# Kernel tuning notes

Measured on AMD Instinct MI355X. Metric: run time of the kernel, lower is better.

The kernel has to match this reference:

```python
import jax, jax.numpy as jnp
import numpy as np
import math

B, N = 512, 32
OBS, NA = 128, 16
OA = OBS + NA  # 144
DK = 64


def setup_inputs() -> dict:
    key = jax.random.key(0)
    ks = jax.random.split(key, 12)
    return {
        "states": jax.random.normal(ks[0], (B, N, OBS), jnp.float32),
        "policies": jax.random.uniform(ks[1], (B, N, NA), jnp.float32),
        "actions": jax.random.uniform(ks[2], (B, N, NA), jnp.float32),
        "W_obs": jax.random.normal(ks[3], (64, OBS), jnp.float32) * 0.05,
        "b_obs": jax.random.normal(ks[4], (64,), jnp.float32) * 0.05,
        "W_oa": jax.random.normal(ks[5], (64, OA), jnp.float32) * 0.05,
        "b_oa": jax.random.normal(ks[6], (64,), jnp.float32) * 0.05,
        "W_key": jax.random.normal(ks[7], (DK, 64), jnp.float32) * 0.05,
        "W_query": jax.random.normal(ks[8], (DK, 64), jnp.float32) * 0.05,
        "W_attn_val": jax.random.normal(ks[9], (64, 64), jnp.float32) * 0.05,
        "W_f1": jax.random.normal(ks[10], (64, 64), jnp.float32) * 0.05,
        "W_f2": jax.random.normal(ks[11], (16, 64), jnp.float32) * 0.05,
    }


def reference(states, policies, actions, W_obs, b_obs, W_oa, b_oa,
              W_key, W_query, W_attn_val, W_f1, W_f2):
    num_agents = states.shape[1]
    d_k = W_attn_val.shape[0]  # d_k_obs == obs_act_output_dim

    obs_actions = jnp.concatenate([states, actions], axis=-1)   # [B,N,OA]
    obs_policy = jnp.concatenate([states, policies], axis=-1)   # [B,N,OA]

    states_embed = jax.nn.relu(states @ W_obs.T + b_obs)        # [B,N,64]
    key_obs = states_embed @ W_key.T                            # [B,N,DK]
    query_obs = states_embed @ W_query.T                        # [B,N,DK]

    # score after transpose(1,2): score[b,j,i] = q_i . k_j ; softmax over i
    score = jnp.einsum('bid,bjd->bji', query_obs, key_obs)
    weight = jax.nn.softmax(score / math.sqrt(d_k), axis=-1)    # [B,N,N]

    # mixed input: for row j, entry i uses policy if i==j else action
    eye = jnp.eye(num_agents, dtype=states.dtype)[None, :, :, None]  # [1,N,N,1]
    oap = eye * obs_policy[:, None, :, :] + (1.0 - eye) * obs_actions[:, None, :, :]  # [B,N,N,OA]

    emb = jax.nn.relu(oap @ W_oa.T + b_oa)                      # [B,N,N,64]
    attn_vals = jnp.tanh(emb @ W_attn_val.T)                    # [B,N,N,64]

    node_features = jnp.mean(attn_vals * weight[..., None], axis=2)  # [B,N,64]

    value = jax.nn.leaky_relu(node_features @ W_f1.T)           # slope 0.01, matches torch default
    value = value @ W_f2.T                                      # [B,N,16]
    return value, weight
```

## Files before the change

kernel.cpp:

```cpp
#include <hip/hip_runtime.h>

typedef _Float16 f16;
typedef _Float16 f16x8 __attribute__((ext_vector_type(8)));
typedef float f32x4 __attribute__((ext_vector_type(4)));

#define MFMA16(a, b, c) __builtin_amdgcn_mfma_f32_16x16x32_f16((a), (b), (c), 0, 0, 0)

#define WS_OBS 0
#define WS_OA  16384
#define WS_K   36864
#define WS_Q   45056
#define WS_AV  53248
#define WS_F1  61440
#define WS_F2  69632
#define WS_TOT 71680

#define XS_HI  0
#define XS_LO  4352
#define E_HI   8704
#define E_LO   11008
#define EA_HI  13312
#define EA_LO  15616
#define EP_HI  17920
#define EP_LO  20224
#define KB_HI  22528
#define KB_LO  24832
#define QB_HI  27136
#define QB_LO  29440
#define AAT_HI 31744
#define AAT_LO 34304
#define WM_HI  36864
#define WM_LO  38144
#define WDIAG  39424
#define SMTOT  39488

__device__ __forceinline__ void split1(float v, ushort& h, ushort& lo) {
    f16 hf = (f16)v;
    float r = v - (float)hf;
    f16 lf = (f16)r;
    union { f16 f; ushort u; } a, b;
    a.f = hf; b.f = lf;
    h = a.u; lo = b.u;
}
__device__ __forceinline__ void split4(f32x4 v, ushort4& h, ushort4& l) {
    split1(v[0], h.x, l.x);
    split1(v[1], h.y, l.y);
    split1(v[2], h.z, l.z);
    split1(v[3], h.w, l.w);
}
__device__ __forceinline__ void mk8(float4 a, float4 b, f16x8& hi, f16x8& lo) {
    float v[8] = {a.x, a.y, a.z, a.w, b.x, b.y, b.z, b.w};
    #pragma unroll
    for (int j = 0; j < 8; ++j) {
        f16 h = (f16)v[j];
        hi[j] = h;
        lo[j] = (f16)(v[j] - (float)h);
    }
}
__device__ __forceinline__ f16x8 ldf(const ushort* sm, int off) {
    return *(const f16x8*)(sm + off);
}
__device__ __forceinline__ f16x8 ldw(const f16* wsf, int base, int psz, int nch,
                                     int p, int nt, int c, int l) {
    return *(const f16x8*)(wsf + base + p * psz + (((nt * nch + c) << 6) + l) * 8);
}
__device__ __forceinline__ float fast_tanh(float x) {
    float xc = fminf(fmaxf(x, -9.0f), 9.0f);
    float e = __expf(2.0f * xc);
    return (e - 1.0f) * __builtin_amdgcn_rcpf(e + 1.0f);
}

__global__ void prep_frags(const float* __restrict__ Wobs, const float* __restrict__ Woa,
                           const float* __restrict__ Wk,   const float* __restrict__ Wq,
                           const float* __restrict__ Wav,  const float* __restrict__ Wf1,
                           const float* __restrict__ Wf2,  f16* __restrict__ wsf) {
    int tid = blockIdx.x * 256 + threadIdx.x;
    if (tid >= 8960) return;
    int p = tid >= 4480 ? 1 : 0;
    int g = tid - p * 4480;
    const float* W; int base, psz, nch, Kreal, g0;
    if (g < 1024)      { W = Wobs; base = WS_OBS; psz = 8192;  nch = 4; Kreal = 128; g0 = g; }
    else if (g < 2304) { W = Woa;  base = WS_OA;  psz = 10240; nch = 5; Kreal = 144; g0 = g - 1024; }
    else if (g < 2816) { W = Wk;   base = WS_K;   psz = 4096;  nch = 2; Kreal = 64;  g0 = g - 2304; }
    else if (g < 3328) { W = Wq;   base = WS_Q;   psz = 4096;  nch = 2; Kreal = 64;  g0 = g - 2816; }
    else if (g < 3840) { W = Wav;  base = WS_AV;  psz = 4096;  nch = 2; Kreal = 64;  g0 = g - 3328; }
    else if (g < 4352) { W = Wf1;  base = WS_F1;  psz = 4096;  nch = 2; Kreal = 64;  g0 = g - 3840; }
    else               { W = Wf2;  base = WS_F2;  psz = 1024;  nch = 2; Kreal = 64;  g0 = g - 4352; }
    int l = g0 & 63, fc = g0 >> 6;
    int c = fc % nch, nt = fc / nch;
    int o = nt * 16 + (l & 15);
    int k0 = c * 32 + (l >> 4) * 8;
    f16 out[8];
    #pragma unroll
    for (int j = 0; j < 8; ++j) {
        int k = k0 + j;
        float v = (k < Kreal) ? W[o * Kreal + k] : 0.0f;
        f16 h = (f16)v;
        out[j] = p ? (f16)(v - (float)h) : h;
    }
    *(f16x8*)(wsf + base + p * psz + g0 * 8) = *(f16x8*)out;
}

__global__ void __launch_bounds__(256, 2)
critic_mfma(const float* __restrict__ states, const float* __restrict__ policies,
            const float* __restrict__ actions, const float* __restrict__ b_obs,
            const float* __restrict__ b_oa, const f16* __restrict__ wsf,
            float* __restrict__ out_value,
            float* __restrict__ out_weight)
{
    __shared__ ushort sm[SMTOT];
    const int b = blockIdx.x;
    const int t = threadIdx.x;
    const int wv = t >> 6, l = t & 63;
    const int lr = l & 15;
    const int lg = l >> 4;
    const int ft = wv;
    const int f0 = ft * 16 + lg * 4;

    float4 sv[4];
    {
        const float4* src = (const float4*)(states + (size_t)b * 4096);
        #pragma unroll
        for (int r4 = 0; r4 < 4; ++r4) sv[r4] = src[t + r4 * 256];
    }

    f16x8 wObsH[4], wObsL[4], wOaH[4], wOaL[4];
    #pragma unroll
    for (int c = 0; c < 4; ++c) {
        wObsH[c] = ldw(wsf, WS_OBS, 8192, 4, 0, ft, c, l);
        wObsL[c] = ldw(wsf, WS_OBS, 8192, 4, 1, ft, c, l);
        wOaH[c]  = ldw(wsf, WS_OA, 10240, 5, 0, ft, c, l);
        wOaL[c]  = ldw(wsf, WS_OA, 10240, 5, 1, ft, c, l);
    }
    f16x8 wTailH = ldw(wsf, WS_OA, 10240, 5, 0, ft, 4, l);
    f16x8 wTailL = ldw(wsf, WS_OA, 10240, 5, 1, ft, 4, l);

    f16x8 actH[2], actL[2], polH[2], polL[2];
    #pragma unroll
    for (int at = 0; at < 2; ++at) {
        float4 a0v = make_float4(0.f, 0.f, 0.f, 0.f), a1v = a0v, p0v = a0v, p1v = a0v;
        if (lg < 2) {
            size_t base = (size_t)b * 512 + (at * 16 + lr) * 16 + lg * 8;
            a0v = *(const float4*)(actions + base);
            a1v = *(const float4*)(actions + base + 4);
            p0v = *(const float4*)(policies + base);
            p1v = *(const float4*)(policies + base + 4);
        }
        mk8(a0v, a1v, actH[at], actL[at]);
        mk8(p0v, p1v, polH[at], polL[at]);
    }

    #pragma unroll
    for (int r4 = 0; r4 < 4; ++r4) {
        int e4 = t + r4 * 256, row = e4 >> 5, k0 = (e4 & 31) * 4;
        ushort4 h, lo;
        split1(sv[r4].x, h.x, lo.x);
        split1(sv[r4].y, h.y, lo.y);
        split1(sv[r4].z, h.z, lo.z);
        split1(sv[r4].w, h.w, lo.w);
        *(ushort4*)(sm + XS_HI + row * 136 + k0) = h;
        *(ushort4*)(sm + XS_LO + row * 136 + k0) = lo;
    }
    __syncthreads();

    const f32x4 Z = {0.f, 0.f, 0.f, 0.f};

    f32x4 accE[2] = {Z, Z}, accP[2] = {Z, Z};
    #pragma unroll
    for (int c = 0; c < 4; ++c) {
        #pragma unroll
        for (int at = 0; at < 2; ++at) {
            int ao = (at * 16 + lr) * 136 + c * 32 + lg * 8;
            f16x8 xh = ldf(sm, XS_HI + ao), xl = ldf(sm, XS_LO + ao);
            accE[at] = MFMA16(wObsH[c], xh, accE[at]);
            accE[at] = MFMA16(wObsH[c], xl, accE[at]);
            accE[at] = MFMA16(wObsL[c], xh, accE[at]);
            accP[at] = MFMA16(wOaH[c], xh, accP[at]);
            accP[at] = MFMA16(wOaH[c], xl, accP[at]);
            accP[at] = MFMA16(wOaL[c], xh, accP[at]);
        }
    }
    f32x4 accEA[2], accEP[2];
    #pragma unroll
    for (int at = 0; at < 2; ++at) {
        accEA[at] = accP[at]; accEP[at] = accP[at];
        accEA[at] = MFMA16(wTailH, actH[at], accEA[at]);
        accEA[at] = MFMA16(wTailH, actL[at], accEA[at]);
        accEA[at] = MFMA16(wTailL, actH[at], accEA[at]);
        accEP[at] = MFMA16(wTailH, polH[at], accEP[at]);
        accEP[at] = MFMA16(wTailH, polL[at], accEP[at]);
        accEP[at] = MFMA16(wTailL, polH[at], accEP[at]);
    }

    f16x8 wKH[2], wKL[2], wQH[2], wQL[2], wVH[2], wVL[2];
    #pragma unroll
    for (int c = 0; c < 2; ++c) {
        wKH[c] = ldw(wsf, WS_K, 4096, 2, 0, ft, c, l);
        wKL[c] = ldw(wsf, WS_K, 4096, 2, 1, ft, c, l);
        wQH[c] = ldw(wsf, WS_Q, 4096, 2, 0, ft, c, l);
        wQL[c] = ldw(wsf, WS_Q, 4096, 2, 1, ft, c, l);
        wVH[c] = ldw(wsf, WS_AV, 4096, 2, 0, ft, c, l);
        wVL[c] = ldw(wsf, WS_AV, 4096, 2, 1, ft, c, l);
    }

    {
        float4 bo = *(const float4*)&b_obs[f0];
        float4 ba = *(const float4*)&b_oa[f0];
        #pragma unroll
        for (int at = 0; at < 2; ++at) {
            int agent = at * 16 + lr;
            f32x4 e, ea, ep;
            e[0] = fmaxf(accE[at][0] + bo.x, 0.f);  e[1] = fmaxf(accE[at][1] + bo.y, 0.f);
            e[2] = fmaxf(accE[at][2] + bo.z, 0.f);  e[3] = fmaxf(accE[at][3] + bo.w, 0.f);
            ea[0] = fmaxf(accEA[at][0] + ba.x, 0.f); ea[1] = fmaxf(accEA[at][1] + ba.y, 0.f);
            ea[2] = fmaxf(accEA[at][2] + ba.z, 0.f); ea[3] = fmaxf(accEA[at][3] + ba.w, 0.f);
            ep[0] = fmaxf(accEP[at][0] + ba.x, 0.f); ep[1] = fmaxf(accEP[at][1] + ba.y, 0.f);
            ep[2] = fmaxf(accEP[at][2] + ba.z, 0.f); ep[3] = fmaxf(accEP[at][3] + ba.w, 0.f);
            ushort4 h, lo;
            split4(e, h, lo);
            *(ushort4*)(sm + E_HI + agent * 72 + f0) = h;
            *(ushort4*)(sm + E_LO + agent * 72 + f0) = lo;
            split4(ea, h, lo);
            *(ushort4*)(sm + EA_HI + agent * 72 + f0) = h;
            *(ushort4*)(sm + EA_LO + agent * 72 + f0) = lo;
            split4(ep, h, lo);
            *(ushort4*)(sm + EP_HI + agent * 72 + f0) = h;
            *(ushort4*)(sm + EP_LO + agent * 72 + f0) = lo;
        }
    }
    __syncthreads();

    f32x4 dDiff[2];
    {
        f32x4 aK[2] = {Z, Z}, aQ[2] = {Z, Z}, aA[2] = {Z, Z}, aP[2] = {Z, Z};
        #pragma unroll
        for (int c = 0; c < 2; ++c) {
            #pragma unroll
            for (int at = 0; at < 2; ++at) {
                int ao = (at * 16 + lr) * 72 + c * 32 + lg * 8;
                f16x8 eh = ldf(sm, E_HI + ao),  el = ldf(sm, E_LO + ao);
                f16x8 xh = ldf(sm, EA_HI + ao), xl = ldf(sm, EA_LO + ao);
                f16x8 yh = ldf(sm, EP_HI + ao), yl = ldf(sm, EP_LO + ao);
                aK[at] = MFMA16(wKH[c], eh, aK[at]);
                aK[at] = MFMA16(wKH[c], el, aK[at]);
                aK[at] = MFMA16(wKL[c], eh, aK[at]);
                aQ[at] = MFMA16(wQH[c], eh, aQ[at]);
                aQ[at] = MFMA16(wQH[c], el, aQ[at]);
                aQ[at] = MFMA16(wQL[c], eh, aQ[at]);
                aA[at] = MFMA16(wVH[c], xh, aA[at]);
                aA[at] = MFMA16(wVH[c], xl, aA[at]);
                aA[at] = MFMA16(wVL[c], xh, aA[at]);
                aP[at] = MFMA16(wVH[c], yh, aP[at]);
                aP[at] = MFMA16(wVH[c], yl, aP[at]);
                aP[at] = MFMA16(wVL[c], yh, aP[at]);
            }
        }
        #pragma unroll
        for (int at = 0; at < 2; ++at) {
            int agent = at * 16 + lr;
            ushort4 h, lo;
            split4(aK[at], h, lo);
            *(ushort4*)(sm + KB_HI + agent * 72 + f0) = h;
            *(ushort4*)(sm + KB_LO + agent * 72 + f0) = lo;
            split4(aQ[at], h, lo);
            *(ushort4*)(sm + QB_HI + agent * 72 + f0) = h;
            *(ushort4*)(sm + QB_LO + agent * 72 + f0) = lo;
            f32x4 ta, tp;
            #pragma unroll
            for (int r = 0; r < 4; ++r) {
                ta[r] = fast_tanh(aA[at][r]);
                tp[r] = fast_tanh(aP[at][r]);
            }
            dDiff[at] = tp - ta;
            #pragma unroll
            for (int r = 0; r < 4; ++r) {
                ushort hh, ll;
                split1(ta[r], hh, ll);
                sm[AAT_HI + (f0 + r) * 40 + agent] = hh;
                sm[AAT_LO + (f0 + r) * 40 + agent] = ll;
            }
        }
    }

    f16x8 wF1H[2], wF1L[2], wF2H[2], wF2L[2];
    #pragma unroll
    for (int c = 0; c < 2; ++c) {
        wF1H[c] = ldw(wsf, WS_F1, 4096, 2, 0, ft, c, l);
        wF1L[c] = ldw(wsf, WS_F1, 4096, 2, 1, ft, c, l);
    }
    if (wv < 2) {
        #pragma unroll
        for (int c = 0; c < 2; ++c) {
            wF2H[c] = ldw(wsf, WS_F2, 1024, 2, 0, 0, c, l);
            wF2L[c] = ldw(wsf, WS_F2, 1024, 2, 1, 0, c, l);
        }
    }
    __syncthreads();

    if (wv < 2) {
        int jt = wv;
        f16x8 kh[2], kl[2];
        #pragma unroll
        for (int c = 0; c < 2; ++c) {
            int ko = (jt * 16 + lr) * 72 + c * 32 + lg * 8;
            kh[c] = ldf(sm, KB_HI + ko);
            kl[c] = ldf(sm, KB_LO + ko);
        }
        f32x4 s[2] = {Z, Z};
        #pragma unroll
        for (int c = 0; c < 2; ++c) {
            #pragma unroll
            for (int it = 0; it < 2; ++it) {
                int qo = (it * 16 + lr) * 72 + c * 32 + lg * 8;
                f16x8 qh = ldf(sm, QB_HI + qo), ql = ldf(sm, QB_LO + qo);
                s[it] = MFMA16(kh[c], qh, s[it]);
                s[it] = MFMA16(kh[c], ql, s[it]);
                s[it] = MFMA16(kl[c], qh, s[it]);
            }
        }
        float* wdiag = (float*)(sm + WDIAG);
        #pragma unroll
        for (int r = 0; r < 4; ++r) {
            int j = jt * 16 + lg * 4 + r;
            float v0 = s[0][r] * 0.125f, v1 = s[1][r] * 0.125f;
            float m = fmaxf(v0, v1);
            #pragma unroll
            for (int off = 1; off < 16; off <<= 1)
                m = fmaxf(m, __shfl_xor(m, off, 16));
            float e0 = __expf(v0 - m), e1 = __expf(v1 - m);
            float su = e0 + e1;
            #pragma unroll
            for (int off = 1; off < 16; off <<= 1)
                su += __shfl_xor(su, off, 16);
            float inv = 1.0f / su;
            e0 *= inv; e1 *= inv;
            out_weight[(size_t)b * 1024 + j * 32 + lr] = e0;
            out_weight[(size_t)b * 1024 + j * 32 + 16 + lr] = e1;
            ushort hh, ll;
            split1(e0, hh, ll);
            sm[WM_HI + j * 40 + lr] = hh;
            sm[WM_LO + j * 40 + lr] = ll;
            split1(e1, hh, ll);
            sm[WM_HI + j * 40 + 16 + lr] = hh;
            sm[WM_LO + j * 40 + 16 + lr] = ll;
            if (lr == lg * 4 + r) wdiag[j] = jt ? e1 : e0;
        }
    }
    __syncthreads();

    {
        int fo = (ft * 16 + lr) * 40 + lg * 8;
        f16x8 ah = ldf(sm, AAT_HI + fo);
        f16x8 al = ldf(sm, AAT_LO + fo);
        const float* wdiag = (const float*)(sm + WDIAG);
        #pragma unroll
        for (int jt = 0; jt < 2; ++jt) {
            int j = jt * 16 + lr;
            f16x8 wh = ldf(sm, WM_HI + j * 40 + lg * 8);
            f16x8 wl = ldf(sm, WM_LO + j * 40 + lg * 8);
            f32x4 acc = Z;
            acc = MFMA16(ah, wh, acc);
            acc = MFMA16(ah, wl, acc);
            acc = MFMA16(al, wh, acc);
            float wd = wdiag[j];
            f32x4 nf;
            #pragma unroll
            for (int r = 0; r < 4; ++r)
                nf[r] = (acc[r] + wd * dDiff[jt][r]) * 0.03125f;
            ushort4 h, lo;
            split4(nf, h, lo);
            *(ushort4*)(sm + E_HI + j * 72 + f0) = h;
            *(ushort4*)(sm + E_LO + j * 72 + f0) = lo;
        }
    }
    __syncthreads();

    {
        f32x4 hA[2] = {Z, Z};
        #pragma unroll
        for (int c = 0; c < 2; ++c) {
            #pragma unroll
            for (int jt = 0; jt < 2; ++jt) {
                int bo2 = (jt * 16 + lr) * 72 + c * 32 + lg * 8;
                f16x8 nh_ = ldf(sm, E_HI + bo2), nl_ = ldf(sm, E_LO + bo2);
                hA[jt] = MFMA16(wF1H[c], nh_, hA[jt]);
                hA[jt] = MFMA16(wF1H[c], nl_, hA[jt]);
                hA[jt] = MFMA16(wF1L[c], nh_, hA[jt]);
            }
        }
        #pragma unroll
        for (int jt = 0; jt < 2; ++jt) {
            int j = jt * 16 + lr;
            f32x4 hv;
            #pragma unroll
            for (int r = 0; r < 4; ++r)
                hv[r] = fmaxf(hA[jt][r], 0.01f * hA[jt][r]);
            ushort4 h, lo;
            split4(hv, h, lo);
            *(ushort4*)(sm + EA_HI + j * 72 + f0) = h;
            *(ushort4*)(sm + EA_LO + j * 72 + f0) = lo;
        }
    }
    __syncthreads();

    if (wv < 2) {
        int jt = wv;
        f32x4 acc = Z;
        #pragma unroll
        for (int c = 0; c < 2; ++c) {
            int ho = (jt * 16 + lr) * 72 + c * 32 + lg * 8;
            f16x8 hh = ldf(sm, EA_HI + ho), hl = ldf(sm, EA_LO + ho);
            acc = MFMA16(wF2H[c], hh, acc);
            acc = MFMA16(wF2H[c], hl, acc);
            acc = MFMA16(wF2L[c], hh, acc);
        }
        int j = jt * 16 + lr;
        *(float4*)&out_value[(size_t)b * 512 + j * 16 + lg * 4] =
            make_float4(acc[0], acc[1], acc[2], acc[3]);
    }
}

extern "C" void kernel_launch(void* const* d_in, const int* in_sizes, int n_in,
                              void* d_out, int out_size, void* d_ws, size_t ws_size,
                              hipStream_t stream) {
    const float* states   = (const float*)d_in[0];
    const float* policies = (const float*)d_in[1];
    const float* actions  = (const float*)d_in[2];
    const float* W_obs    = (const float*)d_in[3];
    const float* b_obs    = (const float*)d_in[4];
    const float* W_oa     = (const float*)d_in[5];
    const float* b_oa     = (const float*)d_in[6];
    const float* W_key    = (const float*)d_in[7];
    const float* W_query  = (const float*)d_in[8];
    const float* W_av     = (const float*)d_in[9];
    const float* W_f1     = (const float*)d_in[10];
    const float* W_f2     = (const float*)d_in[11];

    f16* wsf = (f16*)d_ws;
    float* out_value  = (float*)d_out;
    float* out_weight = (float*)d_out + 512 * 32 * 16;

    prep_frags<<<35, 256, 0, stream>>>(W_obs, W_oa, W_key, W_query, W_av, W_f1, W_f2, wsf);
    critic_mfma<<<512, 256, 0, stream>>>(states, policies, actions,
                                         b_obs, b_oa, wsf, out_value, out_weight);
}
```

Before: 20.57 us.

## Pack two batch elements per 512-thread block with overlapped LDS arenas

Each block now processes two batch elements, one per 256-thread half, with 256 blocks of 512 threads instead of 512 blocks of 256. The shared-memory layout is reorganised so later buffers (K/Q/AAT etc.) alias the input staging area, shrinking each half's arena. The first projection's MFMA chains are split into two independent accumulators per output to shorten dependency chains. Risks: launch_bounds(512,2) tightens register limits and may cause spills, and block-wide barriers now couple two independent batch items.

```diff
diff --git a/kernel.cpp b/kernel.cpp
--- a/kernel.cpp
+++ b/kernel.cpp
@@ -17,22 +17,23 @@
 
 #define XS_HI  0
 #define XS_LO  4352
-#define E_HI   8704
-#define E_LO   11008
-#define EA_HI  13312
-#define EA_LO  15616
-#define EP_HI  17920
-#define EP_LO  20224
-#define KB_HI  22528
-#define KB_LO  24832
-#define QB_HI  27136
-#define QB_LO  29440
-#define AAT_HI 31744
-#define AAT_LO 34304
-#define WM_HI  36864
-#define WM_LO  38144
-#define WDIAG  39424
-#define SMTOT  39488
+#define KB_HI  0
+#define KB_LO  2304
+#define QB_HI  4608
+#define QB_LO  6912
+#define AAT_HI 9216
+#define AAT_LO 11776
+#define E_HI   14336
+#define E_LO   16640
+#define EA_HI  18944
+#define EA_LO  21248
+#define EP_HI  23552
+#define EP_LO  25856
+#define WM_HI  28160
+#define WM_LO  29440
+#define WDIAG  30720
+#define ARENA  30784
+#define SMTOT  (2 * ARENA)
 
 __device__ __forceinline__ void split1(float v, ushort& h, ushort& lo) {
     f16 hf = (f16)v;
@@ -101,27 +102,30 @@
     *(f16x8*)(wsf + base + p * psz + g0 * 8) = *(f16x8*)out;
 }
 
-__global__ void __launch_bounds__(256, 2)
+__global__ void __launch_bounds__(512, 2)
 critic_mfma(const float* __restrict__ states, const float* __restrict__ policies,
             const float* __restrict__ actions, const float* __restrict__ b_obs,
             const float* __restrict__ b_oa, const f16* __restrict__ wsf,
             float* __restrict__ out_value,
             float* __restrict__ out_weight)
 {
-    __shared__ ushort sm[SMTOT];
-    const int b = blockIdx.x;
+    __shared__ ushort smraw[SMTOT];
     const int t = threadIdx.x;
     const int wv = t >> 6, l = t & 63;
+    const int bt = t >> 8;
+    const int tb = t & 255;
+    const int ft = wv & 3;
     const int lr = l & 15;
     const int lg = l >> 4;
-    const int ft = wv;
     const int f0 = ft * 16 + lg * 4;
+    const int b = blockIdx.x * 2 + bt;
+    ushort* sm = smraw + bt * ARENA;
 
     float4 sv[4];
     {
         const float4* src = (const float4*)(states + (size_t)b * 4096);
         #pragma unroll
-        for (int r4 = 0; r4 < 4; ++r4) sv[r4] = src[t + r4 * 256];
+        for (int r4 = 0; r4 < 4; ++r4) sv[r4] = src[tb + r4 * 256];
     }
 
     f16x8 wObsH[4], wObsL[4], wOaH[4], wOaL[4];
@@ -152,7 +156,7 @@
 
     #pragma unroll
     for (int r4 = 0; r4 < 4; ++r4) {
-        int e4 = t + r4 * 256, row = e4 >> 5, k0 = (e4 & 31) * 4;
+        int e4 = tb + r4 * 256, row = e4 >> 5, k0 = (e4 & 31) * 4;
         ushort4 h, lo;
         split1(sv[r4].x, h.x, lo.x);
         split1(sv[r4].y, h.y, lo.y);
@@ -165,25 +169,37 @@
 
     const f32x4 Z = {0.f, 0.f, 0.f, 0.f};
 
-    f32x4 accE[2] = {Z, Z}, accP[2] = {Z, Z};
+    f32x4 accEa[2] = {Z, Z}, accEb[2] = {Z, Z}, accPa[2] = {Z, Z}, accPb[2] = {Z, Z};
     #pragma unroll
     for (int c = 0; c < 4; ++c) {
         #pragma unroll
         for (int at = 0; at < 2; ++at) {
             int ao = (at * 16 + lr) * 136 + c * 32 + lg * 8;
             f16x8 xh = ldf(sm, XS_HI + ao), xl = ldf(sm, XS_LO + ao);
-            accE[at] = MFMA16(wObsH[c], xh, accE[at]);
-            accE[at] = MFMA16(wObsH[c], xl, accE[at]);
-            accE[at] = MFMA16(wObsL[c], xh, accE[at]);
-            accP[at] = MFMA16(wOaH[c], xh, accP[at]);
-            accP[at] = MFMA16(wOaH[c], xl, accP[at]);
-            accP[at] = MFMA16(wOaL[c], xh, accP[at]);
-        }
-    }
-    f32x4 accEA[2], accEP[2];
+            if ((c & 1) == 0) {
+                accEa[at] = MFMA16(wObsH[c], xh, accEa[at]);
+                accEa[at] = MFMA16(wObsH[c], xl, accEa[at]);
+                accEa[at] = MFMA16(wObsL[c], xh, accEa[at]);
+                accPa[at] = MFMA16(wOaH[c], xh, accPa[at]);
+                accPa[at] = MFMA16(wOaH[c], xl, accPa[at]);
+                accPa[at] = MFMA16(wOaL[c], xh, accPa[at]);
+            } else {
+                accEb[at] = MFMA16(wObsH[c], xh, accEb[at]);
+                accEb[at] = MFMA16(wObsH[c], xl, accEb[at]);
+                accEb[at] = MFMA16(wObsL[c], xh, accEb[at]);
+                accPb[at] = MFMA16(wOaH[c], xh, accPb[at]);
+                accPb[at] = MFMA16(wOaH[c], xl, accPb[at]);
+                accPb[at] = MFMA16(wOaL[c], xh, accPb[at]);
+            }
+        }
+    }
+    f32x4 accE[2], accEA[2], accEP[2];
     #pragma unroll
     for (int at = 0; at < 2; ++at) {
-        accEA[at] = accP[at]; accEP[at] = accP[at];
+        accE[at] = accEa[at] + accEb[at];
+        f32x4 base = accPa[at] + accPb[at];
+        accEA[at] = base;
+        accEP[at] = base;
         accEA[at] = MFMA16(wTailH, actH[at], accEA[at]);
         accEA[at] = MFMA16(wTailH, actL[at], accEA[at]);
         accEA[at] = MFMA16(wTailL, actH[at], accEA[at]);
@@ -288,7 +304,7 @@
         wF1H[c] = ldw(wsf, WS_F1, 4096, 2, 0, ft, c, l);
         wF1L[c] = ldw(wsf, WS_F1, 4096, 2, 1, ft, c, l);
     }
-    if (wv < 2) {
+    if (ft < 2) {
         #pragma unroll
         for (int c = 0; c < 2; ++c) {
             wF2H[c] = ldw(wsf, WS_F2, 1024, 2, 0, 0, c, l);
@@ -297,8 +313,8 @@
     }
     __syncthreads();
 
-    if (wv < 2) {
-        int jt = wv;
+    if (ft < 2) {
+        int jt = ft;
         f16x8 kh[2], kl[2];
         #pragma unroll
         for (int c = 0; c < 2; ++c) {
@@ -403,8 +419,8 @@
     }
     __syncthreads();
 
-    if (wv < 2) {
-        int jt = wv;
+    if (ft < 2) {
+        int jt = ft;
         f32x4 acc = Z;
         #pragma unroll
         for (int c = 0; c < 2; ++c) {
@@ -441,6 +457,6 @@
     float* out_weight = (float*)d_out + 512 * 32 * 16;
 
     prep_frags<<<35, 256, 0, stream>>>(W_obs, W_oa, W_key, W_query, W_av, W_f1, W_f2, wsf);
-    critic_mfma<<<512, 256, 0, stream>>>(states, policies, actions,
+    critic_mfma<<<256, 512, 0, stream>>>(states, policies, actions,
                                          b_obs, b_oa, wsf, out_value, out_weight);
 }
```

Result: slower. 21.09 us (+2.5%).

## Merge weight prep into a single-wave-per-batch critic kernel

Applied to the files above, without the earlier changes.

Removes the separate prep_frags launch and instead loads fp32 weights directly in the main kernel, splitting them into hi/lo fp16 fragments on the fly. Each batch element is now handled by one 64-thread wave that loops over the four feature tiles, in place of four waves. States are loaded straight into registers instead of being staged through shared memory, which shrinks LDS use. This trades a kernel launch and several barriers for more serial work per wave, repeated weight conversion in every block, and lower parallelism per block.

```diff
diff --git a/kernel.cpp b/kernel.cpp
--- a/kernel.cpp
+++ b/kernel.cpp
@@ -6,33 +6,22 @@
 
 #define MFMA16(a, b, c) __builtin_amdgcn_mfma_f32_16x16x32_f16((a), (b), (c), 0, 0, 0)
 
-#define WS_OBS 0
-#define WS_OA  16384
-#define WS_K   36864
-#define WS_Q   45056
-#define WS_AV  53248
-#define WS_F1  61440
-#define WS_F2  69632
-#define WS_TOT 71680
-
-#define XS_HI  0
-#define XS_LO  4352
-#define E_HI   8704
-#define E_LO   11008
-#define EA_HI  13312
-#define EA_LO  15616
-#define EP_HI  17920
-#define EP_LO  20224
-#define KB_HI  22528
-#define KB_LO  24832
-#define QB_HI  27136
-#define QB_LO  29440
-#define AAT_HI 31744
-#define AAT_LO 34304
-#define WM_HI  36864
-#define WM_LO  38144
-#define WDIAG  39424
-#define SMTOT  39488
+#define E_HI   0
+#define E_LO   2304
+#define EA_HI  4608
+#define EA_LO  6912
+#define EP_HI  9216
+#define EP_LO  11520
+#define KB_HI  13824
+#define KB_LO  16128
+#define QB_HI  18432
+#define QB_LO  20736
+#define AAT_HI 23040
+#define AAT_LO 25600
+#define WM_HI  28160
+#define WM_LO  29440
+#define WDIAG  30720
+#define SMTOT  30784
 
 __device__ __forceinline__ void split1(float v, ushort& h, ushort& lo) {
     f16 hf = (f16)v;
@@ -57,12 +46,13 @@
         lo[j] = (f16)(v[j] - (float)h);
     }
 }
+__device__ __forceinline__ void ldraw(const float* p, f16x8& h, f16x8& l) {
+    float4 a = *(const float4*)p;
+    float4 b = *(const float4*)(p + 4);
+    mk8(a, b, h, l);
+}
 __device__ __forceinline__ f16x8 ldf(const ushort* sm, int off) {
     return *(const f16x8*)(sm + off);
-}
-__device__ __forceinline__ f16x8 ldw(const f16* wsf, int base, int psz, int nch,
-                                     int p, int nt, int c, int l) {
-    return *(const f16x8*)(wsf + base + p * psz + (((nt * nch + c) << 6) + l) * 8);
 }
 __device__ __forceinline__ float fast_tanh(float x) {
     float xc = fminf(fmaxf(x, -9.0f), 9.0f);
@@ -70,70 +60,31 @@
     return (e - 1.0f) * __builtin_amdgcn_rcpf(e + 1.0f);
 }
 
-__global__ void prep_frags(const float* __restrict__ Wobs, const float* __restrict__ Woa,
-                           const float* __restrict__ Wk,   const float* __restrict__ Wq,
-                           const float* __restrict__ Wav,  const float* __restrict__ Wf1,
-                           const float* __restrict__ Wf2,  f16* __restrict__ wsf) {
-    int tid = blockIdx.x * 256 + threadIdx.x;
-    if (tid >= 8960) return;
-    int p = tid >= 4480 ? 1 : 0;
-    int g = tid - p * 4480;
-    const float* W; int base, psz, nch, Kreal, g0;
-    if (g < 1024)      { W = Wobs; base = WS_OBS; psz = 8192;  nch = 4; Kreal = 128; g0 = g; }
-    else if (g < 2304) { W = Woa;  base = WS_OA;  psz = 10240; nch = 5; Kreal = 144; g0 = g - 1024; }
-    else if (g < 2816) { W = Wk;   base = WS_K;   psz = 4096;  nch = 2; Kreal = 64;  g0 = g - 2304; }
-    else if (g < 3328) { W = Wq;   base = WS_Q;   psz = 4096;  nch = 2; Kreal = 64;  g0 = g - 2816; }
-    else if (g < 3840) { W = Wav;  base = WS_AV;  psz = 4096;  nch = 2; Kreal = 64;  g0 = g - 3328; }
-    else if (g < 4352) { W = Wf1;  base = WS_F1;  psz = 4096;  nch = 2; Kreal = 64;  g0 = g - 3840; }
-    else               { W = Wf2;  base = WS_F2;  psz = 1024;  nch = 2; Kreal = 64;  g0 = g - 4352; }
-    int l = g0 & 63, fc = g0 >> 6;
-    int c = fc % nch, nt = fc / nch;
-    int o = nt * 16 + (l & 15);
-    int k0 = c * 32 + (l >> 4) * 8;
-    f16 out[8];
-    #pragma unroll
-    for (int j = 0; j < 8; ++j) {
-        int k = k0 + j;
-        float v = (k < Kreal) ? W[o * Kreal + k] : 0.0f;
-        f16 h = (f16)v;
-        out[j] = p ? (f16)(v - (float)h) : h;
-    }
-    *(f16x8*)(wsf + base + p * psz + g0 * 8) = *(f16x8*)out;
-}
-
-__global__ void __launch_bounds__(256, 2)
-critic_mfma(const float* __restrict__ states, const float* __restrict__ policies,
-            const float* __restrict__ actions, const float* __restrict__ b_obs,
-            const float* __restrict__ b_oa, const f16* __restrict__ wsf,
-            float* __restrict__ out_value,
-            float* __restrict__ out_weight)
+__global__ void __launch_bounds__(64, 1)
+critic_one(const float* __restrict__ states, const float* __restrict__ policies,
+           const float* __restrict__ actions, const float* __restrict__ b_obs,
+           const float* __restrict__ b_oa,
+           const float* __restrict__ W_obs, const float* __restrict__ W_oa,
+           const float* __restrict__ W_key, const float* __restrict__ W_query,
+           const float* __restrict__ W_av,  const float* __restrict__ W_f1,
+           const float* __restrict__ W_f2,
+           float* __restrict__ out_value,
+           float* __restrict__ out_weight)
 {
     __shared__ ushort sm[SMTOT];
     const int b = blockIdx.x;
-    const int t = threadIdx.x;
-    const int wv = t >> 6, l = t & 63;
+    const int l = threadIdx.x;
     const int lr = l & 15;
     const int lg = l >> 4;
-    const int ft = wv;
-    const int f0 = ft * 16 + lg * 4;
-
-    float4 sv[4];
-    {
-        const float4* src = (const float4*)(states + (size_t)b * 4096);
-        #pragma unroll
-        for (int r4 = 0; r4 < 4; ++r4) sv[r4] = src[t + r4 * 256];
-    }
-
-    f16x8 wObsH[4], wObsL[4], wOaH[4], wOaL[4];
-    #pragma unroll
-    for (int c = 0; c < 4; ++c) {
-        wObsH[c] = ldw(wsf, WS_OBS, 8192, 4, 0, ft, c, l);
-        wObsL[c] = ldw(wsf, WS_OBS, 8192, 4, 1, ft, c, l);
-        wOaH[c]  = ldw(wsf, WS_OA, 10240, 5, 0, ft, c, l);
-        wOaL[c]  = ldw(wsf, WS_OA, 10240, 5, 1, ft, c, l);
-    }
-    f16x8 wTailH = ldw(wsf, WS_OA, 10240, 5, 0, ft, 4, l);
-    f16x8 wTailL = ldw(wsf, WS_OA, 10240, 5, 1, ft, 4, l);
+    const f32x4 Z = {0.f, 0.f, 0.f, 0.f};
+
+    f16x8 sxh[2][4], sxl[2][4];
+    #pragma unroll
+    for (int at = 0; at < 2; ++at)
+        #pragma unroll
+        for (int c = 0; c < 4; ++c)
+            ldraw(states + (size_t)b * 4096 + (at * 16 + lr) * 128 + c * 32 + lg * 8,
+                  sxh[at][c], sxl[at][c]);
 
     f16x8 actH[2], actL[2], polH[2], polL[2];
     #pragma unroll
@@ -151,71 +102,56 @@
     }
 
     #pragma unroll
-    for (int r4 = 0; r4 < 4; ++r4) {
-        int e4 = t + r4 * 256, row = e4 >> 5, k0 = (e4 & 31) * 4;
-        ushort4 h, lo;
-        split1(sv[r4].x, h.x, lo.x);
-        split1(sv[r4].y, h.y, lo.y);
-        split1(sv[r4].z, h.z, lo.z);
-        split1(sv[r4].w, h.w, lo.w);
-        *(ushort4*)(sm + XS_HI + row * 136 + k0) = h;
-        *(ushort4*)(sm + XS_LO + row * 136 + k0) = lo;
-    }
-    __syncthreads();
-
-    const f32x4 Z = {0.f, 0.f, 0.f, 0.f};
-
-    f32x4 accE[2] = {Z, Z}, accP[2] = {Z, Z};
-    #pragma unroll
-    for (int c = 0; c < 4; ++c) {
-        #pragma unroll
-        for (int at = 0; at < 2; ++at) {
-            int ao = (at * 16 + lr) * 136 + c * 32 + lg * 8;
-            f16x8 xh = ldf(sm, XS_HI + ao), xl = ldf(sm, XS_LO + ao);
-            accE[at] = MFMA16(wObsH[c], xh, accE[at]);
-            accE[at] = MFMA16(wObsH[c], xl, accE[at]);
-            accE[at] = MFMA16(wObsL[c], xh, accE[at]);
-            accP[at] = MFMA16(wOaH[c], xh, accP[at]);
-            accP[at] = MFMA16(wOaH[c], xl, accP[at]);
-            accP[at] = MFMA16(wOaL[c], xh, accP[at]);
-        }
-    }
-    f32x4 accEA[2], accEP[2];
-    #pragma unroll
-    for (int at = 0; at < 2; ++at) {
-        accEA[at] = accP[at]; accEP[at] = accP[at];
-        accEA[at] = MFMA16(wTailH, actH[at], accEA[at]);
-        accEA[at] = MFMA16(wTailH, actL[at], accEA[at]);
-        accEA[at] = MFMA16(wTailL, actH[at], accEA[at]);
-        accEP[at] = MFMA16(wTailH, polH[at], accEP[at]);
-        accEP[at] = MFMA16(wTailH, polL[at], accEP[at]);
-        accEP[at] = MFMA16(wTailL, polH[at], accEP[at]);
-    }
-
-    f16x8 wKH[2], wKL[2], wQH[2], wQL[2], wVH[2], wVL[2];
-    #pragma unroll
-    for (int c = 0; c < 2; ++c) {
-        wKH[c] = ldw(wsf, WS_K, 4096, 2, 0, ft, c, l);
-        wKL[c] = ldw(wsf, WS_K, 4096, 2, 1, ft, c, l);
-        wQH[c] = ldw(wsf, WS_Q, 4096, 2, 0, ft, c, l);
-        wQL[c] = ldw(wsf, WS_Q, 4096, 2, 1, ft, c, l);
-        wVH[c] = ldw(wsf, WS_AV, 4096, 2, 0, ft, c, l);
-        wVL[c] = ldw(wsf, WS_AV, 4096, 2, 1, ft, c, l);
-    }
-
-    {
+    for (int ft = 0; ft < 4; ++ft) {
+        const int row = ft * 16 + lr;
+        const int f0 = ft * 16 + lg * 4;
+        f16x8 oh[4], ol[4], ah[4], al[4];
+        #pragma unroll
+        for (int c = 0; c < 4; ++c) {
+            ldraw(W_obs + row * 128 + c * 32 + lg * 8, oh[c], ol[c]);
+            ldraw(W_oa + row * 144 + c * 32 + lg * 8, ah[c], al[c]);
+        }
+        f16x8 th, tl;
+        {
+            float4 t0 = make_float4(0.f, 0.f, 0.f, 0.f), t1 = t0;
+            if (lg < 2) {
+                t0 = *(const float4*)(W_oa + row * 144 + 128 + lg * 8);
+                t1 = *(const float4*)(W_oa + row * 144 + 132 + lg * 8);
+            }
+            mk8(t0, t1, th, tl);
+        }
+        f32x4 accE[2] = {Z, Z}, accP[2] = {Z, Z};
+        #pragma unroll
+        for (int c = 0; c < 4; ++c) {
+            #pragma unroll
+            for (int at = 0; at < 2; ++at) {
+                accE[at] = MFMA16(oh[c], sxh[at][c], accE[at]);
+                accE[at] = MFMA16(oh[c], sxl[at][c], accE[at]);
+                accE[at] = MFMA16(ol[c], sxh[at][c], accE[at]);
+                accP[at] = MFMA16(ah[c], sxh[at][c], accP[at]);
+                accP[at] = MFMA16(ah[c], sxl[at][c], accP[at]);
+                accP[at] = MFMA16(al[c], sxh[at][c], accP[at]);
+            }
+        }
         float4 bo = *(const float4*)&b_obs[f0];
         float4 ba = *(const float4*)&b_oa[f0];
         #pragma unroll
         for (int at = 0; at < 2; ++at) {
+            f32x4 accA = accP[at], accQ = accP[at];
+            accA = MFMA16(th, actH[at], accA);
+            accA = MFMA16(th, actL[at], accA);
+            accA = MFMA16(tl, actH[at], accA);
+            accQ = MFMA16(th, polH[at], accQ);
+            accQ = MFMA16(th, polL[at], accQ);
+            accQ = MFMA16(tl, polH[at], accQ);
             int agent = at * 16 + lr;
             f32x4 e, ea, ep;
             e[0] = fmaxf(accE[at][0] + bo.x, 0.f);  e[1] = fmaxf(accE[at][1] + bo.y, 0.f);
             e[2] = fmaxf(accE[at][2] + bo.z, 0.f);  e[3] = fmaxf(accE[at][3] + bo.w, 0.f);
-            ea[0] = fmaxf(accEA[at][0] + ba.x, 0.f); ea[1] = fmaxf(accEA[at][1] + ba.y, 0.f);
-            ea[2] = fmaxf(accEA[at][2] + ba.z, 0.f); ea[3] = fmaxf(accEA[at][3] + ba.w, 0.f);
-            ep[0] = fmaxf(accEP[at][0] + ba.x, 0.f); ep[1] = fmaxf(accEP[at][1] + ba.y, 0.f);
-            ep[2] = fmaxf(accEP[at][2] + ba.z, 0.f); ep[3] = fmaxf(accEP[at][3] + ba.w, 0.f);
+            ea[0] = fmaxf(accA[0] + ba.x, 0.f); ea[1] = fmaxf(accA[1] + ba.y, 0.f);
+            ea[2] = fmaxf(accA[2] + ba.z, 0.f); ea[3] = fmaxf(accA[3] + ba.w, 0.f);
+            ep[0] = fmaxf(accQ[0] + ba.x, 0.f); ep[1] = fmaxf(accQ[1] + ba.y, 0.f);
+            ep[2] = fmaxf(accQ[2] + ba.z, 0.f); ep[3] = fmaxf(accQ[3] + ba.w, 0.f);
             ushort4 h, lo;
             split4(e, h, lo);
             *(ushort4*)(sm + E_HI + agent * 72 + f0) = h;
@@ -230,29 +166,46 @@
     }
     __syncthreads();
 
-    f32x4 dDiff[2];
-    {
+    f16x8 beh[2][2], bel[2][2], bxh[2][2], bxl[2][2], byh[2][2], byl[2][2];
+    #pragma unroll
+    for (int at = 0; at < 2; ++at)
+        #pragma unroll
+        for (int c = 0; c < 2; ++c) {
+            int ao = (at * 16 + lr) * 72 + c * 32 + lg * 8;
+            beh[at][c] = ldf(sm, E_HI + ao);  bel[at][c] = ldf(sm, E_LO + ao);
+            bxh[at][c] = ldf(sm, EA_HI + ao); bxl[at][c] = ldf(sm, EA_LO + ao);
+            byh[at][c] = ldf(sm, EP_HI + ao); byl[at][c] = ldf(sm, EP_LO + ao);
+        }
+
+    f32x4 dDiff[4][2];
+    #pragma unroll
+    for (int ft = 0; ft < 4; ++ft) {
+        const int row = ft * 16 + lr;
+        const int f0 = ft * 16 + lg * 4;
+        f16x8 kh[2], kl[2], qh[2], ql[2], vh[2], vl[2];
+        #pragma unroll
+        for (int c = 0; c < 2; ++c) {
+            ldraw(W_key + row * 64 + c * 32 + lg * 8, kh[c], kl[c]);
+            ldraw(W_query + row * 64 + c * 32 + lg * 8, qh[c], ql[c]);
+            ldraw(W_av + row * 64 + c * 32 + lg * 8, vh[c], vl[c]);
+        }
         f32x4 aK[2] = {Z, Z}, aQ[2] = {Z, Z}, aA[2] = {Z, Z}, aP[2] = {Z, Z};
         #pragma unroll
         for (int c = 0; c < 2; ++c) {
             #pragma unroll
             for (int at = 0; at < 2; ++at) {
-                int ao = (at * 16 + lr) * 72 + c * 32 + lg * 8;
-                f16x8 eh = ldf(sm, E_HI + ao),  el = ldf(sm, E_LO + ao);
-                f16x8 xh = ldf(sm, EA_HI + ao), xl = ldf(sm, EA_LO + ao);
-                f16x8 yh = ldf(sm, EP_HI + ao), yl = ldf(sm, EP_LO + ao);
-                aK[at] = MFMA16(wKH[c], eh, aK[at]);
-                aK[at] = MFMA16(wKH[c], el, aK[at]);
-                aK[at] = MFMA16(wKL[c], eh, aK[at]);
-                aQ[at] = MFMA16(wQH[c], eh, aQ[at]);
-                aQ[at] = MFMA16(wQH[c], el, aQ[at]);
-                aQ[at] = MFMA16(wQL[c], eh, aQ[at]);
-                aA[at] = MFMA16(wVH[c], xh, aA[at]);
-                aA[at] = MFMA16(wVH[c], xl, aA[at]);
-                aA[at] = MFMA16(wVL[c], xh, aA[at]);
-                aP[at] = MFMA16(wVH[c], yh, aP[at]);
-                aP[at] = MFMA16(wVH[c], yl, aP[at]);
-                aP[at] = MFMA16(wVL[c], yh, aP[at]);
+                aK[at] = MFMA16(kh[c], beh[at][c], aK[at]);
+                aK[at] = MFMA16(kh[c], bel[at][c], aK[at]);
+                aK[at] = MFMA16(kl[c], beh[at][c], aK[at]);
+                aQ[at] = MFMA16(qh[c], beh[at][c], aQ[at]);
+                aQ[at] = MFMA16(qh[c], bel[at][c], aQ[at]);
+                aQ[at] = MFMA16(ql[c], beh[at][c], aQ[at]);
+                aA[at] = MFMA16(vh[c], bxh[at][c], aA[at]);
+                aA[at] = MFMA16(vh[c], bxl[at][c], aA[at]);
+                aA[at] = MFMA16(vl[c], bxh[at][c], aA[at]);
+                aP[at] = MFMA16(vh[c], byh[at][c], aP[at]);
+                aP[at] = MFMA16(vh[c], byl[at][c], aP[at]);
+                aP[at] = MFMA16(vl[c], byh[at][c], aP[at]);
             }
         }
         #pragma unroll
@@ -271,7 +224,7 @@
                 ta[r] = fast_tanh(aA[at][r]);
                 tp[r] = fast_tanh(aP[at][r]);
             }
-            dDiff[at] = tp - ta;
+            dDiff[ft][at] = tp - ta;
             #pragma unroll
             for (int r = 0; r < 4; ++r) {
                 ushort hh, ll;
@@ -281,142 +234,161 @@
             }
         }
     }
-
-    f16x8 wF1H[2], wF1L[2], wF2H[2], wF2L[2];
-    #pragma unroll
-    for (int c = 0; c < 2; ++c) {
-        wF1H[c] = ldw(wsf, WS_F1, 4096, 2, 0, ft, c, l);
-        wF1L[c] = ldw(wsf, WS_F1, 4096, 2, 1, ft, c, l);
-    }
-    if (wv < 2) {
-        #pragma unroll
-        for (int c = 0; c < 2; ++c) {
-            wF2H[c] = ldw(wsf, WS_F2, 1024, 2, 0, 0, c, l);
-            wF2L[c] = ldw(wsf, WS_F2, 1024, 2, 1, 0, c, l);
-        }
-    }
     __syncthreads();
 
-    if (wv < 2) {
-        int jt = wv;
-        f16x8 kh[2], kl[2];
-        #pragma unroll
-        for (int c = 0; c < 2; ++c) {
-            int ko = (jt * 16 + lr) * 72 + c * 32 + lg * 8;
-            kh[c] = ldf(sm, KB_HI + ko);
-            kl[c] = ldf(sm, KB_LO + ko);
-        }
-        f32x4 s[2] = {Z, Z};
-        #pragma unroll
-        for (int c = 0; c < 2; ++c) {
-            #pragma unroll
-            for (int it = 0; it < 2; ++it) {
-                int qo = (it * 16 + lr) * 72 + c * 32 + lg * 8;
-                f16x8 qh = ldf(sm, QB_HI + qo), ql = ldf(sm, QB_LO + qo);
-                s[it] = MFMA16(kh[c], qh, s[it]);
-                s[it] = MFMA16(kh[c], ql, s[it]);
-                s[it] = MFMA16(kl[c], qh, s[it]);
-            }
-        }
+    {
         float* wdiag = (float*)(sm + WDIAG);
         #pragma unroll
-        for (int r = 0; r < 4; ++r) {
-            int j = jt * 16 + lg * 4 + r;
-            float v0 = s[0][r] * 0.125f, v1 = s[1][r] * 0.125f;
-            float m = fmaxf(v0, v1);
-            #pragma unroll
-            for (int off = 1; off < 16; off <<= 1)
-                m = fmaxf(m, __shfl_xor(m, off, 16));
-            float e0 = __expf(v0 - m), e1 = __expf(v1 - m);
-            float su = e0 + e1;
-            #pragma unroll
-            for (int off = 1; off < 16; off <<= 1)
-                su += __shfl_xor(su, off, 16);
-            float inv = 1.0f / su;
-            e0 *= inv; e1 *= inv;
-            out_weight[(size_t)b * 1024 + j * 32 + lr] = e0;
-            out_weight[(size_t)b * 1024 + j * 32 + 16 + lr] = e1;
-            ushort hh, ll;
-            split1(e0, hh, ll);
-            sm[WM_HI + j * 40 + lr] = hh;
-            sm[WM_LO + j * 40 + lr] = ll;
-            split1(e1, hh, ll);
-            sm[WM_HI + j * 40 + 16 + lr] = hh;
-            sm[WM_LO + j * 40 + 16 + lr] = ll;
-            if (lr == lg * 4 + r) wdiag[j] = jt ? e1 : e0;
+        for (int jt = 0; jt < 2; ++jt) {
+            f16x8 kh[2], kl[2];
+            #pragma unroll
+            for (int c = 0; c < 2; ++c) {
+                int ko = (jt * 16 + lr) * 72 + c * 32 + lg * 8;
+                kh[c] = ldf(sm, KB_HI + ko);
+                kl[c] = ldf(sm, KB_LO + ko);
+            }
+            f32x4 s[2] = {Z, Z};
+            #pragma unroll
+            for (int c = 0; c < 2; ++c) {
+                #pragma unroll
+                for (int it = 0; it < 2; ++it) {
+                    int qo = (it * 16 + lr) * 72 + c * 32 + lg * 8;
+                    f16x8 qh = ldf(sm, QB_HI + qo), ql = ldf(sm, QB_LO + qo);
+                    s[it] = MFMA16(kh[c], qh, s[it]);
+                    s[it] = MFMA16(kh[c], ql, s[it]);
+                    s[it] = MFMA16(kl[c], qh, s[it]);
+                }
+            }
+            #pragma unroll
+            for (int r = 0; r < 4; ++r) {
+                int j = jt * 16 + lg * 4 + r;
+                float v0 = s[0][r] * 0.125f, v1 = s[1][r] * 0.125f;
+                float m = fmaxf(v0, v1);
+                #pragma unroll
+                for (int off = 1; off < 16; off <<= 1)
+                    m = fmaxf(m, __shfl_xor(m, off, 16));
+                float e0 = __expf(v0 - m), e1 = __expf(v1 - m);
+                float su = e0 + e1;
+                #pragma unroll
+                for (int off = 1; off < 16; off <<= 1)
+                    su += __shfl_xor(su, off, 16);
+                float inv = 1.0f / su;
+                e0 *= inv; e1 *= inv;
+                out_weight[(size_t)b * 1024 + j * 32 + lr] = e0;
+                out_weight[(size_t)b * 1024 + j * 32 + 16 + lr] = e1;
+                ushort hh, ll;
+                split1(e0, hh, ll);
+                sm[WM_HI + j * 40 + lr] = hh;
+                sm[WM_LO + j * 40 + lr] = ll;
+                split1(e1, hh, ll);
+                sm[WM_HI + j * 40 + 16 + lr] = hh;
+                sm[WM_LO + j * 40 + 16 + lr] = ll;
+                if (lr == lg * 4 + r) wdiag[j] = jt ? e1 : e0;
+            }
         }
     }
     __syncthreads();
 
     {
-        int fo = (ft * 16 + lr) * 40 + lg * 8;
-        f16x8 ah = ldf(sm, AAT_HI + fo);
-        f16x8 al = ldf(sm, AAT_LO + fo);
         const float* wdiag = (const float*)(sm + WDIAG);
+        f16x8 wh[2], wl[2];
+        float wd[2];
         #pragma unroll
         for (int jt = 0; jt < 2; ++jt) {
             int j = jt * 16 + lr;
-            f16x8 wh = ldf(sm, WM_HI + j * 40 + lg * 8);
-            f16x8 wl = ldf(sm, WM_LO + j * 40 + lg * 8);
+            wh[jt] = ldf(sm, WM_HI + j * 40 + lg * 8);
+            wl[jt] = ldf(sm, WM_LO + j * 40 + lg * 8);
+            wd[jt] = wdiag[j];
+        }
+        #pragma unroll
+        for (int ft = 0; ft < 4; ++ft) {
+            const int f0 = ft * 16 + lg * 4;
+            int fo = (ft * 16 + lr) * 40 + lg * 8;
+            f16x8 ah = ldf(sm, AAT_HI + fo);
+            f16x8 al = ldf(sm, AAT_LO + fo);
+            #pragma unroll
+            for (int jt = 0; jt < 2; ++jt) {
+                int j = jt * 16 + lr;
+                f32x4 acc = Z;
+                acc = MFMA16(ah, wh[jt], acc);
+                acc = MFMA16(ah, wl[jt], acc);
+                acc = MFMA16(al, wh[jt], acc);
+                f32x4 nf;
+                #pragma unroll
+                for (int r = 0; r < 4; ++r)
+                    nf[r] = (acc[r] + wd[jt] * dDiff[ft][jt][r]) * 0.03125f;
+                ushort4 h, lo;
+                split4(nf, h, lo);
+                *(ushort4*)(sm + E_HI + j * 72 + f0) = h;
+                *(ushort4*)(sm + E_LO + j * 72 + f0) = lo;
+            }
+        }
+    }
+    __syncthreads();
+
+    {
+        f16x8 nfh[2][2], nfl[2][2];
+        #pragma unroll
+        for (int jt = 0; jt < 2; ++jt)
+            #pragma unroll
+            for (int c = 0; c < 2; ++c) {
+                int no = (jt * 16 + lr) * 72 + c * 32 + lg * 8;
+                nfh[jt][c] = ldf(sm, E_HI + no);
+                nfl[jt][c] = ldf(sm, E_LO + no);
+            }
+        #pragma unroll
+        for (int ft = 0; ft < 4; ++ft) {
+            const int row = ft * 16 + lr;
+            const int f0 = ft * 16 + lg * 4;
+            f16x8 w1h[2], w1l[2];
+            #pragma unroll
+            for (int c = 0; c < 2; ++c)
+                ldraw(W_f1 + row * 64 + c * 32 + lg * 8, w1h[c], w1l[c]);
+            f32x4 hA[2] = {Z, Z};
+            #pragma unroll
+            for (int c = 0; c < 2; ++c)
+                #pragma unroll
+                for (int jt = 0; jt < 2; ++jt) {
+                    hA[jt] = MFMA16(w1h[c], nfh[jt][c], hA[jt]);
+                    hA[jt] = MFMA16(w1h[c], nfl[jt][c], hA[jt]);
+                    hA[jt] = MFMA16(w1l[c], nfh[jt][c], hA[jt]);
+                }
+            #pragma unroll
+            for (int jt = 0; jt < 2; ++jt) {
+                int j = jt * 16 + lr;
+                f32x4 hv;
+                #pragma unroll
+                for (int r = 0; r < 4; ++r)
+                    hv[r] = fmaxf(hA[jt][r], 0.01f * hA[jt][r]);
+                ushort4 h, lo;
+                split4(hv, h, lo);
+                *(ushort4*)(sm + EA_HI + j * 72 + f0) = h;
+                *(ushort4*)(sm + EA_LO + j * 72 + f0) = lo;
+            }
+        }
+    }
+    __syncthreads();
+
+    {
+        f16x8 w2h[2], w2l[2];
+        #pragma unroll
+        for (int c = 0; c < 2; ++c)
+            ldraw(W_f2 + lr * 64 + c * 32 + lg * 8, w2h[c], w2l[c]);
+        #pragma unroll
+        for (int jt = 0; jt < 2; ++jt) {
             f32x4 acc = Z;
-            acc = MFMA16(ah, wh, acc);
-            acc = MFMA16(ah, wl, acc);
-            acc = MFMA16(al, wh, acc);
-            float wd = wdiag[j];
-            f32x4 nf;
-            #pragma unroll
-            for (int r = 0; r < 4; ++r)
-                nf[r] = (acc[r] + wd * dDiff[jt][r]) * 0.03125f;
-            ushort4 h, lo;
-            split4(nf, h, lo);
-            *(ushort4*)(sm + E_HI + j * 72 + f0) = h;
-            *(ushort4*)(sm + E_LO + j * 72 + f0) = lo;
-        }
-    }
-    __syncthreads();
-
-    {
-        f32x4 hA[2] = {Z, Z};
-        #pragma unroll
-        for (int c = 0; c < 2; ++c) {
-            #pragma unroll
-            for (int jt = 0; jt < 2; ++jt) {
-                int bo2 = (jt * 16 + lr) * 72 + c * 32 + lg * 8;
-                f16x8 nh_ = ldf(sm, E_HI + bo2), nl_ = ldf(sm, E_LO + bo2);
-                hA[jt] = MFMA16(wF1H[c], nh_, hA[jt]);
-                hA[jt] = MFMA16(wF1H[c], nl_, hA[jt]);
-                hA[jt] = MFMA16(wF1L[c], nh_, hA[jt]);
-            }
-        }
-        #pragma unroll
-        for (int jt = 0; jt < 2; ++jt) {
+            #pragma unroll
+            for (int c = 0; c < 2; ++c) {
+                int ho = (jt * 16 + lr) * 72 + c * 32 + lg * 8;
+                f16x8 hh = ldf(sm, EA_HI + ho), hl = ldf(sm, EA_LO + ho);
+                acc = MFMA16(w2h[c], hh, acc);
+                acc = MFMA16(w2h[c], hl, acc);
+                acc = MFMA16(w2l[c], hh, acc);
+            }
             int j = jt * 16 + lr;
-            f32x4 hv;
-            #pragma unroll
-            for (int r = 0; r < 4; ++r)
-                hv[r] = fmaxf(hA[jt][r], 0.01f * hA[jt][r]);
-            ushort4 h, lo;
-            split4(hv, h, lo);
-            *(ushort4*)(sm + EA_HI + j * 72 + f0) = h;
-            *(ushort4*)(sm + EA_LO + j * 72 + f0) = lo;
-        }
-    }
-    __syncthreads();
-
-    if (wv < 2) {
-        int jt = wv;
-        f32x4 acc = Z;
-        #pragma unroll
-        for (int c = 0; c < 2; ++c) {
-            int ho = (jt * 16 + lr) * 72 + c * 32 + lg * 8;
-            f16x8 hh = ldf(sm, EA_HI + ho), hl = ldf(sm, EA_LO + ho);
-            acc = MFMA16(wF2H[c], hh, acc);
-            acc = MFMA16(wF2H[c], hl, acc);
-            acc = MFMA16(wF2L[c], hh, acc);
-        }
-        int j = jt * 16 + lr;
-        *(float4*)&out_value[(size_t)b * 512 + j * 16 + lg * 4] =
-            make_float4(acc[0], acc[1], acc[2], acc[3]);
+            *(float4*)&out_value[(size_t)b * 512 + j * 16 + lg * 4] =
+                make_float4(acc[0], acc[1], acc[2], acc[3]);
+        }
     }
 }
 
@@ -436,11 +408,10 @@
     const float* W_f1     = (const float*)d_in[10];
     const float* W_f2     = (const float*)d_in[11];
 
-    f16* wsf = (f16*)d_ws;
     float* out_value  = (float*)d_out;
     float* out_weight = (float*)d_out + 512 * 32 * 16;
 
-    prep_frags<<<35, 256, 0, stream>>>(W_obs, W_oa, W_key, W_query, W_av, W_f1, W_f2, wsf);
-    critic_mfma<<<512, 256, 0, stream>>>(states, policies, actions,
-                                         b_obs, b_oa, wsf, out_value, out_weight);
-}
+    critic_one<<<512, 64, 0, stream>>>(states, policies, actions, b_obs, b_oa,
+                                       W_obs, W_oa, W_key, W_query, W_av, W_f1, W_f2,
+                                       out_value, out_weight);
+}
```

Result: slower. 26.14 us (+27.0%).
